# Kernel tuning notes

Hardware: AMD Instinct MI355X
Metric: run time of the kernel (lower is better)

Reference implementation:

```python
import jax, jax.numpy as jnp
import numpy as np

TEMPERATURE = 0.5
EPS = 1e-20


def setup_inputs() -> dict:
    key = jax.random.key(0)
    ks = jax.random.split(key, 7)
    N, T, S = 16, 64, 1024
    SRC, TGT, D = 512, 512, 64
    return {
        "input": jax.random.normal(ks[0], (N, T, TGT), jnp.float32),
        "memory_bank": jax.random.normal(ks[1], (N, S, SRC), jnp.float32),
        "W_q": jax.random.normal(ks[2], (TGT, D), jnp.float32) / np.sqrt(TGT),
        "W_ctx": jax.random.normal(ks[3], (SRC, D), jnp.float32) / np.sqrt(SRC),
        "v": jax.random.normal(ks[4], (D,), jnp.float32) / np.sqrt(D),
        "W_out": jax.random.normal(ks[5], (SRC + TGT, TGT), jnp.float32) / np.sqrt(SRC + TGT),
        "b_out": jax.random.normal(ks[6], (TGT,), jnp.float32) * 0.01,
    }


def reference(input, memory_bank, W_q, W_ctx, v, W_out, b_out):
    # MLP attention score: v^T tanh(W_q q + W_ctx h)
    wq = jnp.einsum("ntd,de->nte", input, W_q)            # [N,T,D]
    uh = jnp.einsum("nsd,de->nse", memory_bank, W_ctx)    # [N,S,D]
    wquh = jnp.tanh(wq[:, :, None, :] + uh[:, None, :, :])  # [N,T,S,D]
    scores = jnp.einsum("ntsd,d->nts", wquh, v)           # [N,T,S]

    log_alpha = jax.nn.log_softmax(scores, axis=-1)
    alpha = jnp.exp(log_alpha)                            # c_align_vectors

    # deterministic context + output
    context_c = jnp.einsum("nts,nsd->ntd", alpha, memory_bank)
    h_c = jnp.tanh(jnp.concatenate([input, context_c], axis=-1) @ W_out + b_out)

    # gumbel-softmax sample (K = n_samples = 1, forced by view_as in original)
    u = jax.random.uniform(jax.random.key(42), log_alpha.shape, jnp.float32)
    g = -jnp.log(-jnp.log(u + EPS) + EPS)                 # gumbel noise
    y_align = jax.nn.softmax((log_alpha + g) / TEMPERATURE, axis=-1)  # [N,T,S]

    context_y = jnp.einsum("nts,nsd->ntd", y_align, memory_bank)
    h_y = jnp.tanh(jnp.concatenate([input, context_y], axis=-1) @ W_out + b_out)

    return jnp.stack([h_c, h_y], axis=0)  # [2,N,T,tgt_dim]
```

## Files before the change

### kernel.cpp

```cpp
#include <hip/hip_runtime.h>
#include <hip/hip_bf16.h>
#include <stdint.h>

#define DEV __device__ __forceinline__

typedef __attribute__((ext_vector_type(8))) short short8;
typedef __attribute__((ext_vector_type(4))) float f32x4;

#define TWO_LOG2E 2.8853900817779268f

DEV unsigned short f2bf(float f) {
  uint32_t u = __float_as_uint(f);
  u += 0x7FFFu + ((u >> 16) & 1u);
  return (unsigned short)(u >> 16);
}

DEV uint2 pk4(float4 f) {
  union { __hip_bfloat162 h; unsigned u; } a, b;
  a.h = __float22bfloat162_rn(make_float2(f.x, f.y));
  b.h = __float22bfloat162_rn(make_float2(f.z, f.w));
  return make_uint2(a.u, b.u);
}

DEV short8 mk8(uint2 lo, uint2 hi) {
  union { short8 s; uint4 u; } t;
  t.u = make_uint4(lo.x, lo.y, hi.x, hi.y);
  return t.s;
}

DEV uint32_t rotl32(uint32_t x, int r) { return (x << r) | (x >> (32 - r)); }

DEV void threefry_0_42(uint32_t x0, uint32_t x1, uint32_t& o0, uint32_t& o1) {
  const uint32_t ks0 = 0u, ks1 = 42u, ks2 = 0x1BD11BDAu ^ 42u;
  x0 += ks0; x1 += ks1;
#define TFR(r) { x0 += x1; x1 = rotl32(x1, (r)); x1 ^= x0; }
  TFR(13) TFR(15) TFR(26) TFR(6)  x0 += ks1; x1 += ks2 + 1u;
  TFR(17) TFR(29) TFR(16) TFR(24) x0 += ks2; x1 += ks0 + 2u;
  TFR(13) TFR(15) TFR(26) TFR(6)  x0 += ks0; x1 += ks1 + 3u;
  TFR(17) TFR(29) TFR(16) TFR(24) x0 += ks1; x1 += ks2 + 4u;
  TFR(13) TFR(15) TFR(26) TFR(6)  x0 += ks2; x1 += ks0 + 5u;
#undef TFR
  o0 = x0; o1 = x1;
}

DEV float wredmax(float v) {
#pragma unroll
  for (int off = 32; off > 0; off >>= 1) v = fmaxf(v, __shfl_xor(v, off));
  return v;
}
DEV float wredsum(float v) {
#pragma unroll
  for (int off = 32; off > 0; off >>= 1) v += __shfl_xor(v, off);
  return v;
}

DEV void ph_transpose(int b, int tid, char* smem,
                      const float* Wctx, const float* Wq, const float* Wout,
                      unsigned short* WctxT, unsigned short* WqT, unsigned short* WoutT) {
  float (*tile)[65] = (float(*)[65])smem;
  const float* src; unsigned short* dst; int R, C, br, bc;
  if (b < 8)       { src = Wctx; dst = WctxT; R = 512;  C = 64;  br = b * 64;       bc = 0; }
  else if (b < 16) { src = Wq;   dst = WqT;   R = 512;  C = 64;  br = (b - 8) * 64; bc = 0; }
  else { int i = b - 16; src = Wout; dst = WoutT; R = 1024; C = 512; br = (i & 15) * 64; bc = (i >> 4) * 64; }
  const int lr = tid >> 4, lc4 = (tid & 15) * 4;
#pragma unroll
  for (int i = 0; i < 4; ++i) {
    float4 vv = *(const float4*)(src + (long)(br + lr + i * 16) * C + bc + lc4);
    tile[lr + i * 16][lc4 + 0] = vv.x;
    tile[lr + i * 16][lc4 + 1] = vv.y;
    tile[lr + i * 16][lc4 + 2] = vv.z;
    tile[lr + i * 16][lc4 + 3] = vv.w;
  }
  __syncthreads();
#pragma unroll
  for (int i = 0; i < 4; ++i) {
    int crow = lr + i * 16;
    ushort4 o;
    o.x = f2bf(tile[lc4 + 0][crow]);
    o.y = f2bf(tile[lc4 + 1][crow]);
    o.z = f2bf(tile[lc4 + 2][crow]);
    o.w = f2bf(tile[lc4 + 3][crow]);
    *(ushort4*)(dst + (long)(bc + crow) * R + br + lc4) = o;
  }
}

DEV void ph_mbtile(int i, int tid, char* smem, const float* mb, unsigned short* mbT) {
  float (*tile)[65] = (float(*)[65])smem;
  const int n = i >> 7, rem = i & 127;
  const int sr0 = (rem >> 3) * 64;
  const int c0 = (rem & 7) * 64;
  const int lr = tid >> 4, lc4 = (tid & 15) * 4;
#pragma unroll
  for (int k = 0; k < 4; ++k) {
    float4 vv = *(const float4*)(mb + ((long)n * 1024 + sr0 + lr + k * 16) * 512 + c0 + lc4);
    tile[lr + k * 16][lc4 + 0] = vv.x;
    tile[lr + k * 16][lc4 + 1] = vv.y;
    tile[lr + k * 16][lc4 + 2] = vv.z;
    tile[lr + k * 16][lc4 + 3] = vv.w;
  }
  __syncthreads();
#pragma unroll
  for (int k = 0; k < 4; ++k) {
    int crow = lr + k * 16;
    ushort4 o;
    o.x = f2bf(tile[lc4 + 0][crow]);
    o.y = f2bf(tile[lc4 + 1][crow]);
    o.z = f2bf(tile[lc4 + 2][crow]);
    o.w = f2bf(tile[lc4 + 3][crow]);
    *(ushort4*)(mbT + (long)n * 524288 + (long)(c0 + crow) * 1024 + sr0 + lc4) = o;
  }
}

DEV void ph_uhwq(int t, int tid, char* smem,
                 const float* mb, const float* input,
                 const unsigned short* WctxT, const unsigned short* WqT,
                 float* uhT, float* wqo) {
  unsigned short (*As)[32] = (unsigned short(*)[32])smem;
  unsigned short (*Bs)[32] = (unsigned short(*)[32])(smem + 4096);
  const float* A; const unsigned short* BT; int mbase;
  if (t < 256) { A = mb;    BT = WctxT; mbase = t * 64; }
  else         { A = input; BT = WqT;   mbase = (t - 256) * 64; }
  const int srow = tid >> 2, kc = tid & 3;
  const int scol = ((kc ^ (srow & 3)) * 8);
  const int wave = tid >> 6, lane = tid & 63;
  const int wm = (wave >> 1) * 32, wn = (wave & 1) * 32;
  const int q = lane >> 4, r = lane & 15;
  const int c0 = ((q ^ (r & 3)) * 8);
  const float* ap = A + (long)(mbase + srow) * 512 + kc * 8;
  const unsigned short* bp = BT + (long)srow * 512 + kc * 8;
  f32x4 acc[2][2];
#pragma unroll
  for (int i = 0; i < 2; ++i)
#pragma unroll
    for (int j = 0; j < 2; ++j) acc[i][j] = (f32x4){0.f, 0.f, 0.f, 0.f};
  float4 fa0 = *(const float4*)(ap);
  float4 fa1 = *(const float4*)(ap + 4);
  uint4 fb = *(const uint4*)(bp);
  for (int k0 = 0; k0 < 512; k0 += 32) {
    uint2 p0 = pk4(fa0), p1 = pk4(fa1);
    *(uint4*)&As[srow][scol] = make_uint4(p0.x, p0.y, p1.x, p1.y);
    *(uint4*)&Bs[srow][scol] = fb;
    __syncthreads();
    if (k0 + 32 < 512) {
      fa0 = *(const float4*)(ap + k0 + 32);
      fa1 = *(const float4*)(ap + k0 + 36);
      fb = *(const uint4*)(bp + k0 + 32);
    }
    short8 a0 = *(const short8*)&As[wm + r][c0];
    short8 a1 = *(const short8*)&As[wm + 16 + r][c0];
    short8 b0 = *(const short8*)&Bs[wn + r][c0];
    short8 b1 = *(const short8*)&Bs[wn + 16 + r][c0];
    acc[0][0] = __builtin_amdgcn_mfma_f32_16x16x32_bf16(a0, b0, acc[0][0], 0, 0, 0);
    acc[0][1] = __builtin_amdgcn_mfma_f32_16x16x32_bf16(a0, b1, acc[0][1], 0, 0, 0);
    acc[1][0] = __builtin_amdgcn_mfma_f32_16x16x32_bf16(a1, b0, acc[1][0], 0, 0, 0);
    acc[1][1] = __builtin_amdgcn_mfma_f32_16x16x32_bf16(a1, b1, acc[1][1], 0, 0, 0);
    __syncthreads();
  }
#pragma unroll
  for (int i2 = 0; i2 < 2; ++i2)
#pragma unroll
    for (int j2 = 0; j2 < 2; ++j2) {
      int gcol = wn + j2 * 16 + r;
      int m = mbase + wm + i2 * 16 + q * 4;
      if (t < 256) {
        int n = m >> 10, s0 = m & 1023;
        float4 o;
        o.x = acc[i2][j2][0] * TWO_LOG2E;
        o.y = acc[i2][j2][1] * TWO_LOG2E;
        o.z = acc[i2][j2][2] * TWO_LOG2E;
        o.w = acc[i2][j2][3] * TWO_LOG2E;
        *(float4*)(uhT + (long)n * 65536 + (long)gcol * 1024 + s0) = o;
      } else {
#pragma unroll
        for (int reg = 0; reg < 4; ++reg)
          wqo[(long)(m + reg) * 64 + gcol] = acc[i2][j2][reg] * TWO_LOG2E;
      }
    }
}

DEV void ph_pre(int tt, int tid, char* smem,
                const float* input, const unsigned short* WoutT,
                const float* bout, float* P) {
  unsigned short (*As)[32] = (unsigned short(*)[32])smem;
  unsigned short (*Bs)[32] = (unsigned short(*)[32])(smem + 4096);
  const int mbase = (tt >> 4) * 64, nbase = (tt & 15) * 32;
  const int srow = tid >> 2, kc = tid & 3;
  const int scol = ((kc ^ (srow & 3)) * 8);
  const int wave = tid >> 6, lane = tid & 63;
  const int wm = (wave >> 1) * 32, wn = (wave & 1) * 16;
  const int q = lane >> 4, r = lane & 15;
  const int c0 = ((q ^ (r & 3)) * 8);
  const float* ap = input + (long)(mbase + srow) * 512 + kc * 8;
  const int brow = (tid & 127) >> 2;
  const unsigned short* bp = WoutT + (long)(nbase + brow) * 1024 + kc * 8;
  f32x4 acc[2];
  acc[0] = (f32x4){0.f, 0.f, 0.f, 0.f};
  acc[1] = (f32x4){0.f, 0.f, 0.f, 0.f};
  float4 fa0 = *(const float4*)(ap);
  float4 fa1 = *(const float4*)(ap + 4);
  uint4 fb;
  if (tid < 128) fb = *(const uint4*)(bp);
  for (int k0 = 0; k0 < 512; k0 += 32) {
    uint2 p0 = pk4(fa0), p1 = pk4(fa1);
    *(uint4*)&As[srow][scol] = make_uint4(p0.x, p0.y, p1.x, p1.y);
    if (tid < 128) *(uint4*)&Bs[brow][(kc ^ (brow & 3)) * 8] = fb;
    __syncthreads();
    int kn = k0 + 32;
    if (kn < 512) {
      fa0 = *(const float4*)(ap + kn);
      fa1 = *(const float4*)(ap + kn + 4);
      if (tid < 128) fb = *(const uint4*)(bp + kn);
    }
    short8 a0 = *(const short8*)&As[wm + r][c0];
    short8 a1 = *(const short8*)&As[wm + 16 + r][c0];
    short8 b0 = *(const short8*)&Bs[wn + r][c0];
    acc[0] = __builtin_amdgcn_mfma_f32_16x16x32_bf16(a0, b0, acc[0], 0, 0, 0);
    acc[1] = __builtin_amdgcn_mfma_f32_16x16x32_bf16(a1, b0, acc[1], 0, 0, 0);
    __syncthreads();
  }
#pragma unroll
  for (int i2 = 0; i2 < 2; ++i2) {
    int gcol = nbase + wn + r;
    float bb = bout[gcol];
#pragma unroll
    for (int reg = 0; reg < 4; ++reg) {
      int grow = mbase + wm + i2 * 16 + q * 4 + reg;
      P[(long)grow * 512 + gcol] = acc[i2][reg] + bb;
    }
  }
}

DEV void softmax_gumbel_write(float* lsc, int nt, int tid, float* red,
                              unsigned short* alpha_bf, unsigned short* yal_bf) {
  const int wv = tid >> 6, ln = tid & 63;
  float m = fmaxf(fmaxf(lsc[0], lsc[1]), fmaxf(lsc[2], lsc[3]));
  m = wredmax(m);
  if (ln == 0) red[wv] = m;
  __syncthreads();
  m = fmaxf(fmaxf(red[0], red[1]), fmaxf(red[2], red[3]));
  __syncthreads();
  float ss = 0.f;
#pragma unroll
  for (int i = 0; i < 4; ++i) ss += __expf(lsc[i] - m);
  ss = wredsum(ss);
  if (ln == 0) red[wv] = ss;
  __syncthreads();
  ss = red[0] + red[1] + red[2] + red[3];
  const float logl = __logf(ss);
  __syncthreads();

  const uint32_t jbase = (uint32_t)nt * 1024u + (uint32_t)tid * 4u;
  float ys[4];
  float4 av;
#pragma unroll
  for (int i = 0; i < 4; ++i) {
    float la = lsc[i] - m - logl;
    ((float*)&av)[i] = __expf(la);
    uint32_t o0, o1;
    threefry_0_42(0u, jbase + i, o0, o1);
    uint32_t bits = o0 ^ o1;
    float u = __uint_as_float((bits >> 9) | 0x3f800000u) - 1.0f;
    float g = -__logf(-__logf(u + 1e-20f) + 1e-20f);
    ys[i] = (la + g) * 2.0f;
  }
  {
    uint2 pa = pk4(av);
    *(uint2*)(alpha_bf + (long)nt * 1024 + tid * 4) = pa;
  }
  float m2 = fmaxf(fmaxf(ys[0], ys[1]), fmaxf(ys[2], ys[3]));
  m2 = wredmax(m2);
  if (ln == 0) red[wv] = m2;
  __syncthreads();
  m2 = fmaxf(fmaxf(red[0], red[1]), fmaxf(red[2], red[3]));
  __syncthreads();
  float s2 = 0.f;
  float4 ye;
#pragma unroll
  for (int i = 0; i < 4; ++i) { ((float*)&ye)[i] = __expf(ys[i] - m2); s2 += ((float*)&ye)[i]; }
  s2 = wredsum(s2);
  if (ln == 0) red[wv] = s2;
  __syncthreads();
  s2 = red[0] + red[1] + red[2] + red[3];
  const float rinv = __fdividef(1.f, s2);
  ye.x *= rinv; ye.y *= rinv; ye.z *= rinv; ye.w *= rinv;
  {
    uint2 py = pk4(ye);
    *(uint2*)(yal_bf + (long)nt * 1024 + tid * 4) = py;
  }
  __syncthreads();
}

DEV void ph_scores_pair(int nt0, int tid, char* smem,
                        const float* uhT, const float* wqo, const float* vvec,
                        unsigned short* alpha_bf, unsigned short* yal_bf) {
  float* wvs0 = (float*)smem;
  float* wvs1 = wvs0 + 64;
  float* vvs  = wvs1 + 64;
  float* red  = vvs + 64;
  const int nt1 = nt0 + 512;
  const int n0 = nt0 >> 6, n1 = nt1 >> 6;
  if (tid < 64) {
    wvs0[tid] = wqo[nt0 * 64 + tid];
    wvs1[tid] = wqo[nt1 * 64 + tid];
    vvs[tid]  = vvec[tid];
  }
  __syncthreads();
  float sumv = 0.f;
#pragma unroll
  for (int d = 0; d < 64; d += 4) {
    float4 vv = *(const float4*)&vvs[d];
    sumv += vv.x + vv.y + vv.z + vv.w;
  }
  const float* un0 = uhT + (long)n0 * 65536 + tid * 4;
  const float* un1 = uhT + (long)n1 * 65536 + tid * 4;
  float4 r0 = make_float4(0.f, 0.f, 0.f, 0.f);
  float4 r1 = make_float4(0.f, 0.f, 0.f, 0.f);
  for (int db = 0; db < 64; db += 4) {
    float4 ua[4], ub[4];
#pragma unroll
    for (int j = 0; j < 4; ++j) {
      ua[j] = *(const float4*)(un0 + (long)(db + j) * 1024);
      ub[j] = *(const float4*)(un1 + (long)(db + j) * 1024);
    }
#pragma unroll
    for (int j = 0; j < 4; ++j) {
      float w0 = wvs0[db + j], w1 = wvs1[db + j], vvj = vvs[db + j];
      r0.x = fmaf(vvj, __builtin_amdgcn_rcpf(1.f + __builtin_amdgcn_exp2f(ua[j].x + w0)), r0.x);
      r0.y = fmaf(vvj, __builtin_amdgcn_rcpf(1.f + __builtin_amdgcn_exp2f(ua[j].y + w0)), r0.y);
      r0.z = fmaf(vvj, __builtin_amdgcn_rcpf(1.f + __builtin_amdgcn_exp2f(ua[j].z + w0)), r0.z);
      r0.w = fmaf(vvj, __builtin_amdgcn_rcpf(1.f + __builtin_amdgcn_exp2f(ua[j].w + w0)), r0.w);
      r1.x = fmaf(vvj, __builtin_amdgcn_rcpf(1.f + __builtin_amdgcn_exp2f(ub[j].x + w1)), r1.x);
      r1.y = fmaf(vvj, __builtin_amdgcn_rcpf(1.f + __builtin_amdgcn_exp2f(ub[j].y + w1)), r1.y);
      r1.z = fmaf(vvj, __builtin_amdgcn_rcpf(1.f + __builtin_amdgcn_exp2f(ub[j].z + w1)), r1.z);
      r1.w = fmaf(vvj, __builtin_amdgcn_rcpf(1.f + __builtin_amdgcn_exp2f(ub[j].w + w1)), r1.w);
    }
  }
  float lsc0[4], lsc1[4];
  lsc0[0] = fmaf(-2.f, r0.x, sumv); lsc0[1] = fmaf(-2.f, r0.y, sumv);
  lsc0[2] = fmaf(-2.f, r0.z, sumv); lsc0[3] = fmaf(-2.f, r0.w, sumv);
  lsc1[0] = fmaf(-2.f, r1.x, sumv); lsc1[1] = fmaf(-2.f, r1.y, sumv);
  lsc1[2] = fmaf(-2.f, r1.z, sumv); lsc1[3] = fmaf(-2.f, r1.w, sumv);
  softmax_gumbel_write(lsc0, nt0, tid, red, alpha_bf, yal_bf);
  softmax_gumbel_write(lsc1, nt1, tid, red, alpha_bf, yal_bf);
}

DEV void ph_ctx_fast(int n, int dbase, int vt, int tid, char* smem,
                     const unsigned short* alpha_bf, const unsigned short* yal_bf,
                     const unsigned short* mbT, unsigned short* ctxb) {
  unsigned short (*As)[32] = (unsigned short(*)[32])smem;
  const int srow = tid >> 2, kc = tid & 3;
  const int scol = ((kc ^ (srow & 3)) * 8);
  const int wave = tid >> 6, lane = tid & 63;
  const int wm = (wave >> 1) * 32, wn = (wave & 1) * 16;
  const int q = lane >> 4, r = lane & 15;
  const int c0 = ((q ^ (r & 3)) * 8);
  const unsigned short* Ab = (vt ? yal_bf : alpha_bf) + (long)n * 65536 + (long)srow * 1024 + kc * 8;
  const unsigned short* Bb = mbT + (long)n * 524288 + (long)(dbase + wn + r) * 1024 + q * 8;
  f32x4 acc[2];
  acc[0] = (f32x4){0.f, 0.f, 0.f, 0.f};
  acc[1] = (f32x4){0.f, 0.f, 0.f, 0.f};
  uint4 fa  = *(const uint4*)(Ab);
  uint4 fb0 = *(const uint4*)(Bb);
  uint4 fb1 = *(const uint4*)(Bb + 32);
  for (int k0 = 0; k0 < 1024; k0 += 32) {
    *(uint4*)&As[srow][scol] = fa;
    __syncthreads();
    union { uint4 u; short8 s; } bu; bu.u = fb0;
    if (k0 + 32 < 1024) fa = *(const uint4*)(Ab + k0 + 32);
    fb0 = fb1;
    if (k0 + 64 < 1024) fb1 = *(const uint4*)(Bb + k0 + 64);
    short8 a0 = *(const short8*)&As[wm + r][c0];
    short8 a1 = *(const short8*)&As[wm + 16 + r][c0];
    acc[0] = __builtin_amdgcn_mfma_f32_16x16x32_bf16(a0, bu.s, acc[0], 0, 0, 0);
    acc[1] = __builtin_amdgcn_mfma_f32_16x16x32_bf16(a1, bu.s, acc[1], 0, 0, 0);
    __syncthreads();
  }
#pragma unroll
  for (int i2 = 0; i2 < 2; ++i2) {
    int gcol = dbase + wn + r;
#pragma unroll
    for (int reg = 0; reg < 4; ++reg) {
      long grow = (long)vt * 1024 + n * 64 + wm + i2 * 16 + q * 4 + reg;
      ctxb[grow * 512 + gcol] = f2bf(acc[i2][reg]);
    }
  }
}

DEV void ph_ctx_legacy(int n, int dbase, int vt, int tid, char* smem,
                       const unsigned short* alpha_bf, const unsigned short* yal_bf,
                       const float* mb, unsigned short* ctxb) {
  unsigned short (*As)[32] = (unsigned short(*)[32])smem;
  const int srow = tid >> 2, kc = tid & 3;
  const int scol = ((kc ^ (srow & 3)) * 8);
  const int wave = tid >> 6, lane = tid & 63;
  const int wm = (wave >> 1) * 32, wn = (wave & 1) * 16;
  const int q = lane >> 4, r = lane & 15;
  const int c0 = ((q ^ (r & 3)) * 8);
  const unsigned short* Ab = (vt ? yal_bf : alpha_bf) + (long)n * 65536 + (long)srow * 1024 + kc * 8;
  const float* bcol = mb + (long)n * 524288 + dbase + wn + r;
  f32x4 acc[2];
  acc[0] = (f32x4){0.f, 0.f, 0.f, 0.f};
  acc[1] = (f32x4){0.f, 0.f, 0.f, 0.f};
  uint4 fa = *(const uint4*)(Ab);
  float bv[8];
#pragma unroll
  for (int j = 0; j < 8; ++j) bv[j] = bcol[(long)(q * 8 + j) * 512];
  for (int k0 = 0; k0 < 1024; k0 += 32) {
    *(uint4*)&As[srow][scol] = fa;
    __syncthreads();
    float4 blo = make_float4(bv[0], bv[1], bv[2], bv[3]);
    float4 bhi = make_float4(bv[4], bv[5], bv[6], bv[7]);
    short8 b0 = mk8(pk4(blo), pk4(bhi));
    if (k0 + 32 < 1024) {
      fa = *(const uint4*)(Ab + k0 + 32);
#pragma unroll
      for (int j = 0; j < 8; ++j) bv[j] = bcol[(long)(k0 + 32 + q * 8 + j) * 512];
    }
    short8 a0 = *(const short8*)&As[wm + r][c0];
    short8 a1 = *(const short8*)&As[wm + 16 + r][c0];
    acc[0] = __builtin_amdgcn_mfma_f32_16x16x32_bf16(a0, b0, acc[0], 0, 0, 0);
    acc[1] = __builtin_amdgcn_mfma_f32_16x16x32_bf16(a1, b0, acc[1], 0, 0, 0);
    __syncthreads();
  }
#pragma unroll
  for (int i2 = 0; i2 < 2; ++i2) {
    int gcol = dbase + wn + r;
#pragma unroll
    for (int reg = 0; reg < 4; ++reg) {
      long grow = (long)vt * 1024 + n * 64 + wm + i2 * 16 + q * 4 + reg;
      ctxb[grow * 512 + gcol] = f2bf(acc[i2][reg]);
    }
  }
}

DEV void ph_out(int mbase, int nbase, int tid, char* smem,
                const unsigned short* ctxb, const unsigned short* WoutT,
                const float* P, float* out) {
  unsigned short (*As)[32] = (unsigned short(*)[32])smem;
  unsigned short (*Bs)[32] = (unsigned short(*)[32])(smem + 4096);
  const int srow = tid >> 2, kc = tid & 3;
  const int scol = ((kc ^ (srow & 3)) * 8);
  const int wave = tid >> 6, lane = tid & 63;
  const int wm = (wave >> 1) * 32, wn = (wave & 1) * 16;
  const int q = lane >> 4, r = lane & 15;
  const int c0 = ((q ^ (r & 3)) * 8);
  const unsigned short* ap = ctxb + (long)(mbase + srow) * 512 + kc * 8;
  const int brow = (tid & 127) >> 2;
  const unsigned short* bp = WoutT + (long)(nbase + brow) * 1024 + 512 + kc * 8;
  f32x4 acc[2];
#pragma unroll
  for (int i2 = 0; i2 < 2; ++i2) {
    int pcol = nbase + wn + r;
#pragma unroll
    for (int reg = 0; reg < 4; ++reg) {
      int prow = (mbase + wm + i2 * 16 + q * 4 + reg) & 1023;
      acc[i2][reg] = P[(long)prow * 512 + pcol];
    }
  }
  uint4 fa = *(const uint4*)(ap);
  uint4 fb;
  if (tid < 128) fb = *(const uint4*)(bp);
  for (int k0 = 0; k0 < 512; k0 += 32) {
    *(uint4*)&As[srow][scol] = fa;
    if (tid < 128) *(uint4*)&Bs[brow][(kc ^ (brow & 3)) * 8] = fb;
    __syncthreads();
    int kn = k0 + 32;
    if (kn < 512) {
      fa = *(const uint4*)(ap + kn);
      if (tid < 128) fb = *(const uint4*)(bp + kn);
    }
    short8 a0 = *(const short8*)&As[wm + r][c0];
    short8 a1 = *(const short8*)&As[wm + 16 + r][c0];
    short8 b0 = *(const short8*)&Bs[wn + r][c0];
    acc[0] = __builtin_amdgcn_mfma_f32_16x16x32_bf16(a0, b0, acc[0], 0, 0, 0);
    acc[1] = __builtin_amdgcn_mfma_f32_16x16x32_bf16(a1, b0, acc[1], 0, 0, 0);
    __syncthreads();
  }
#pragma unroll
  for (int i2 = 0; i2 < 2; ++i2) {
    int gcol = nbase + wn + r;
#pragma unroll
    for (int reg = 0; reg < 4; ++reg) {
      int grow = mbase + wm + i2 * 16 + q * 4 + reg;
      float z = acc[i2][reg];
      float rc = __builtin_amdgcn_rcpf(1.f + __builtin_amdgcn_exp2f(z * TWO_LOG2E));
      out[(long)grow * 512 + gcol] = fmaf(-2.f, rc, 1.f);
    }
  }
}

__global__ __launch_bounds__(256) void k_prep(const float* __restrict__ Wctx,
                                              const float* __restrict__ Wq,
                                              const float* __restrict__ Wout,
                                              const float* __restrict__ mb,
                                              unsigned short* __restrict__ WctxT,
                                              unsigned short* __restrict__ WqT,
                                              unsigned short* __restrict__ WoutT,
                                              unsigned short* __restrict__ mbT) {
  __shared__ __align__(16) char smem[16640];
  const int b = blockIdx.x;
  if (b < 144) ph_transpose(b, threadIdx.x, smem, Wctx, Wq, Wout, WctxT, WqT, WoutT);
  else         ph_mbtile(b - 144, threadIdx.x, smem, mb, mbT);
}

__global__ __launch_bounds__(256) void k_uhwq_pre(const float* __restrict__ mb,
                                                  const float* __restrict__ input,
                                                  const unsigned short* __restrict__ WctxT,
                                                  const unsigned short* __restrict__ WqT,
                                                  const unsigned short* __restrict__ WoutT,
                                                  const float* __restrict__ bout,
                                                  float* __restrict__ uhT,
                                                  float* __restrict__ wqo,
                                                  float* __restrict__ P) {
  __shared__ __align__(16) char smem[8192];
  const int b = blockIdx.x;
  if (b < 272) ph_uhwq(b, threadIdx.x, smem, mb, input, WctxT, WqT, uhT, wqo);
  else         ph_pre(b - 272, threadIdx.x, smem, input, WoutT, bout, P);
}

__global__ __launch_bounds__(256) void k_scores(const float* __restrict__ uhT,
                                                const float* __restrict__ wqo,
                                                const float* __restrict__ vvec,
                                                unsigned short* __restrict__ alpha_bf,
                                                unsigned short* __restrict__ yal_bf) {
  __shared__ __align__(16) char smem[1024];
  ph_scores_pair(blockIdx.x, threadIdx.x, smem, uhT, wqo, vvec, alpha_bf, yal_bf);
}

__global__ __launch_bounds__(256) void k_ctx_fast(const unsigned short* __restrict__ alpha_bf,
                                                  const unsigned short* __restrict__ yal_bf,
                                                  const unsigned short* __restrict__ mbT,
                                                  unsigned short* __restrict__ ctxb) {
  __shared__ __align__(16) char smem[4096];
  const int x = blockIdx.x;
  ph_ctx_fast(x & 15, ((x >> 4) & 15) * 32, x >> 8, threadIdx.x, smem, alpha_bf, yal_bf, mbT, ctxb);
}

__global__ __launch_bounds__(256) void k_ctx_legacy(const unsigned short* __restrict__ alpha_bf,
                                                    const unsigned short* __restrict__ yal_bf,
                                                    const float* __restrict__ mb,
                                                    unsigned short* __restrict__ ctxb) {
  __shared__ __align__(16) char smem[4096];
  const int x = blockIdx.x;
  ph_ctx_legacy(x & 15, ((x >> 4) & 15) * 32, x >> 8, threadIdx.x, smem, alpha_bf, yal_bf, mb, ctxb);
}

__global__ __launch_bounds__(256) void k_out(const unsigned short* __restrict__ ctxb,
                                             const unsigned short* __restrict__ WoutT,
                                             const float* __restrict__ P,
                                             float* __restrict__ out) {
  __shared__ __align__(16) char smem[8192];
  ph_out((blockIdx.x >> 4) * 64, (blockIdx.x & 15) * 32, threadIdx.x, smem, ctxb, WoutT, P, out);
}

extern "C" void kernel_launch(void* const* d_in, const int* in_sizes, int n_in,
                              void* d_out, int out_size, void* d_ws, size_t ws_size,
                              hipStream_t stream) {
  const float* input = (const float*)d_in[0];
  const float* mb    = (const float*)d_in[1];
  const float* W_q   = (const float*)d_in[2];
  const float* W_ctx = (const float*)d_in[3];
  const float* v     = (const float*)d_in[4];
  const float* W_out = (const float*)d_in[5];
  const float* b_out = (const float*)d_in[6];
  float* out = (float*)d_out;
  float* ws = (float*)d_ws;

  float* uhT = ws;
  float* wqo = ws + 1048576;
  unsigned short* alpha_bf = (unsigned short*)(ws + 1114112);
  unsigned short* yal_bf   = (unsigned short*)(ws + 1638400);
  unsigned short* WctxT = (unsigned short*)(ws + 2162688);
  unsigned short* WqT   = (unsigned short*)(ws + 2179072);
  unsigned short* WoutT = (unsigned short*)(ws + 2195456);
  unsigned short* ctxb  = (unsigned short*)(ws + 2457600);
  float* P = ws + 2981888;
  unsigned short* mbT = (unsigned short*)(ws + 3506176);

  const bool big = ws_size >= (size_t)7700480 * 4;

  k_prep<<<big ? 2192 : 144, 256, 0, stream>>>(W_ctx, W_q, W_out, mb, WctxT, WqT, WoutT, mbT);
  k_uhwq_pre<<<528, 256, 0, stream>>>(mb, input, WctxT, WqT, WoutT, b_out, uhT, wqo, P);
  k_scores<<<512, 256, 0, stream>>>(uhT, wqo, v, alpha_bf, yal_bf);
  if (big) k_ctx_fast<<<512, 256, 0, stream>>>(alpha_bf, yal_bf, mbT, ctxb);
  else     k_ctx_legacy<<<512, 256, 0, stream>>>(alpha_bf, yal_bf, mb, ctxb);
  k_out<<<512, 256, 0, stream>>>(ctxb, WoutT, P, out);
}
```

Before: 147.6 us.

## Pre-convert inputs to bf16 and load MFMA fragments directly from global memory

The prep kernel now also writes bf16 copies of memory_bank and input. New GEMM variants for uh/wq, the output pre-projection, the context GEMM and the output GEMM read MFMA operands straight from global memory with register prefetch, replacing the LDS staging and block barriers. The aim is less fp32 traffic and fewer syncs in the GEMM phases. The cost is a larger workspace requirement and more global-memory writes in prep. Without that workspace, the old paths are used.

```diff
diff --git a/kernel.cpp b/kernel.cpp
--- a/kernel.cpp
+++ b/kernel.cpp
@@ -84,7 +84,8 @@
   }
 }
 
-DEV void ph_mbtile(int i, int tid, char* smem, const float* mb, unsigned short* mbT) {
+DEV void ph_mbtile(int i, int tid, char* smem, const float* mb,
+                   unsigned short* mbT, unsigned short* mb_bf) {
   float (*tile)[65] = (float(*)[65])smem;
   const int n = i >> 7, rem = i & 127;
   const int sr0 = (rem >> 3) * 64;
@@ -92,11 +93,15 @@
   const int lr = tid >> 4, lc4 = (tid & 15) * 4;
 #pragma unroll
   for (int k = 0; k < 4; ++k) {
-    float4 vv = *(const float4*)(mb + ((long)n * 1024 + sr0 + lr + k * 16) * 512 + c0 + lc4);
+    const long srow = (long)n * 1024 + sr0 + lr + k * 16;
+    float4 vv = *(const float4*)(mb + srow * 512 + c0 + lc4);
     tile[lr + k * 16][lc4 + 0] = vv.x;
     tile[lr + k * 16][lc4 + 1] = vv.y;
     tile[lr + k * 16][lc4 + 2] = vv.z;
     tile[lr + k * 16][lc4 + 3] = vv.w;
+    ushort4 o;
+    o.x = f2bf(vv.x); o.y = f2bf(vv.y); o.z = f2bf(vv.z); o.w = f2bf(vv.w);
+    *(ushort4*)(mb_bf + srow * 512 + c0 + lc4) = o;
   }
   __syncthreads();
 #pragma unroll
@@ -108,6 +113,197 @@
     o.z = f2bf(tile[lc4 + 2][crow]);
     o.w = f2bf(tile[lc4 + 3][crow]);
     *(ushort4*)(mbT + (long)n * 524288 + (long)(c0 + crow) * 1024 + sr0 + lc4) = o;
+  }
+}
+
+DEV void ph_inpconv(int i, int tid, const float* input, unsigned short* input_bf) {
+  const long base = (long)i * 8192 + (long)tid * 32;
+#pragma unroll
+  for (int j = 0; j < 32; j += 4) {
+    float4 vv = *(const float4*)(input + base + j);
+    uint2 p = pk4(vv);
+    *(uint2*)(input_bf + base + j) = p;
+  }
+}
+
+DEV void ph_uhwq_fast(int t, int tid,
+                      const unsigned short* mb_bf, const unsigned short* input_bf,
+                      const unsigned short* WctxT, const unsigned short* WqT,
+                      float* uhT, float* wqo) {
+  const unsigned short* A; const unsigned short* BT; int mbase;
+  if (t < 256) { A = mb_bf;    BT = WctxT; mbase = t * 64; }
+  else         { A = input_bf; BT = WqT;   mbase = (t - 256) * 64; }
+  const int wave = tid >> 6, lane = tid & 63;
+  const int wm = (wave >> 1) * 32, wn = (wave & 1) * 32;
+  const int q = lane >> 4, r = lane & 15;
+  const unsigned short* a0p = A + (long)(mbase + wm + r) * 512 + q * 8;
+  const unsigned short* a1p = a0p + 16 * 512;
+  const unsigned short* b0p = BT + (long)(wn + r) * 512 + q * 8;
+  const unsigned short* b1p = b0p + 16 * 512;
+  f32x4 acc[2][2];
+#pragma unroll
+  for (int i = 0; i < 2; ++i)
+#pragma unroll
+    for (int j = 0; j < 2; ++j) acc[i][j] = (f32x4){0.f, 0.f, 0.f, 0.f};
+  uint4 na0 = *(const uint4*)(a0p);
+  uint4 na1 = *(const uint4*)(a1p);
+  uint4 nb0 = *(const uint4*)(b0p);
+  uint4 nb1 = *(const uint4*)(b1p);
+  for (int k0 = 0; k0 < 512; k0 += 32) {
+    union { uint4 u; short8 s; } A0, A1, B0, B1;
+    A0.u = na0; A1.u = na1; B0.u = nb0; B1.u = nb1;
+    if (k0 + 32 < 512) {
+      na0 = *(const uint4*)(a0p + k0 + 32);
+      na1 = *(const uint4*)(a1p + k0 + 32);
+      nb0 = *(const uint4*)(b0p + k0 + 32);
+      nb1 = *(const uint4*)(b1p + k0 + 32);
+    }
+    acc[0][0] = __builtin_amdgcn_mfma_f32_16x16x32_bf16(A0.s, B0.s, acc[0][0], 0, 0, 0);
+    acc[0][1] = __builtin_amdgcn_mfma_f32_16x16x32_bf16(A0.s, B1.s, acc[0][1], 0, 0, 0);
+    acc[1][0] = __builtin_amdgcn_mfma_f32_16x16x32_bf16(A1.s, B0.s, acc[1][0], 0, 0, 0);
+    acc[1][1] = __builtin_amdgcn_mfma_f32_16x16x32_bf16(A1.s, B1.s, acc[1][1], 0, 0, 0);
+  }
+#pragma unroll
+  for (int i2 = 0; i2 < 2; ++i2)
+#pragma unroll
+    for (int j2 = 0; j2 < 2; ++j2) {
+      int gcol = wn + j2 * 16 + r;
+      int m = mbase + wm + i2 * 16 + q * 4;
+      if (t < 256) {
+        int n = m >> 10, s0 = m & 1023;
+        float4 o;
+        o.x = acc[i2][j2][0] * TWO_LOG2E;
+        o.y = acc[i2][j2][1] * TWO_LOG2E;
+        o.z = acc[i2][j2][2] * TWO_LOG2E;
+        o.w = acc[i2][j2][3] * TWO_LOG2E;
+        *(float4*)(uhT + (long)n * 65536 + (long)gcol * 1024 + s0) = o;
+      } else {
+#pragma unroll
+        for (int reg = 0; reg < 4; ++reg)
+          wqo[(long)(m + reg) * 64 + gcol] = acc[i2][j2][reg] * TWO_LOG2E;
+      }
+    }
+}
+
+DEV void ph_pre_fast(int tt, int tid, const unsigned short* input_bf,
+                     const unsigned short* WoutT, const float* bout, float* P) {
+  const int mbase = (tt >> 4) * 64, nbase = (tt & 15) * 32;
+  const int wave = tid >> 6, lane = tid & 63;
+  const int wm = (wave >> 1) * 32, wn = (wave & 1) * 16;
+  const int q = lane >> 4, r = lane & 15;
+  const unsigned short* a0p = input_bf + (long)(mbase + wm + r) * 512 + q * 8;
+  const unsigned short* a1p = a0p + 16 * 512;
+  const unsigned short* bp  = WoutT + (long)(nbase + wn + r) * 1024 + q * 8;
+  f32x4 acc[2];
+  acc[0] = (f32x4){0.f, 0.f, 0.f, 0.f};
+  acc[1] = (f32x4){0.f, 0.f, 0.f, 0.f};
+  uint4 na0 = *(const uint4*)(a0p);
+  uint4 na1 = *(const uint4*)(a1p);
+  uint4 nb  = *(const uint4*)(bp);
+  for (int k0 = 0; k0 < 512; k0 += 32) {
+    union { uint4 u; short8 s; } A0, A1, B0;
+    A0.u = na0; A1.u = na1; B0.u = nb;
+    if (k0 + 32 < 512) {
+      na0 = *(const uint4*)(a0p + k0 + 32);
+      na1 = *(const uint4*)(a1p + k0 + 32);
+      nb  = *(const uint4*)(bp + k0 + 32);
+    }
+    acc[0] = __builtin_amdgcn_mfma_f32_16x16x32_bf16(A0.s, B0.s, acc[0], 0, 0, 0);
+    acc[1] = __builtin_amdgcn_mfma_f32_16x16x32_bf16(A1.s, B0.s, acc[1], 0, 0, 0);
+  }
+#pragma unroll
+  for (int i2 = 0; i2 < 2; ++i2) {
+    int gcol = nbase + wn + r;
+    float bb = bout[gcol];
+#pragma unroll
+    for (int reg = 0; reg < 4; ++reg) {
+      int grow = mbase + wm + i2 * 16 + q * 4 + reg;
+      P[(long)grow * 512 + gcol] = acc[i2][reg] + bb;
+    }
+  }
+}
+
+DEV void ph_ctx_fast2(int n, int dbase, int vt, int tid,
+                      const unsigned short* alpha_bf, const unsigned short* yal_bf,
+                      const unsigned short* mbT, unsigned short* ctxb) {
+  const int wave = tid >> 6, lane = tid & 63;
+  const int wm = (wave >> 1) * 32, wn = (wave & 1) * 16;
+  const int q = lane >> 4, r = lane & 15;
+  const unsigned short* Abase = (vt ? yal_bf : alpha_bf) + (long)n * 65536;
+  const unsigned short* a0p = Abase + (long)(wm + r) * 1024 + q * 8;
+  const unsigned short* a1p = a0p + 16 * 1024;
+  const unsigned short* bp  = mbT + (long)n * 524288 + (long)(dbase + wn + r) * 1024 + q * 8;
+  f32x4 acc[2];
+  acc[0] = (f32x4){0.f, 0.f, 0.f, 0.f};
+  acc[1] = (f32x4){0.f, 0.f, 0.f, 0.f};
+  uint4 na0 = *(const uint4*)(a0p);
+  uint4 na1 = *(const uint4*)(a1p);
+  uint4 nb  = *(const uint4*)(bp);
+  for (int k0 = 0; k0 < 1024; k0 += 32) {
+    union { uint4 u; short8 s; } A0, A1, B0;
+    A0.u = na0; A1.u = na1; B0.u = nb;
+    if (k0 + 32 < 1024) {
+      na0 = *(const uint4*)(a0p + k0 + 32);
+      na1 = *(const uint4*)(a1p + k0 + 32);
+      nb  = *(const uint4*)(bp + k0 + 32);
+    }
+    acc[0] = __builtin_amdgcn_mfma_f32_16x16x32_bf16(A0.s, B0.s, acc[0], 0, 0, 0);
+    acc[1] = __builtin_amdgcn_mfma_f32_16x16x32_bf16(A1.s, B0.s, acc[1], 0, 0, 0);
+  }
+#pragma unroll
+  for (int i2 = 0; i2 < 2; ++i2) {
+    int gcol = dbase + wn + r;
+#pragma unroll
+    for (int reg = 0; reg < 4; ++reg) {
+      long grow = (long)vt * 1024 + n * 64 + wm + i2 * 16 + q * 4 + reg;
+      ctxb[grow * 512 + gcol] = f2bf(acc[i2][reg]);
+    }
+  }
+}
+
+DEV void ph_out_fast(int mbase, int nbase, int tid,
+                     const unsigned short* ctxb, const unsigned short* WoutT,
+                     const float* P, float* out) {
+  const int wave = tid >> 6, lane = tid & 63;
+  const int wm = (wave >> 1) * 32, wn = (wave & 1) * 16;
+  const int q = lane >> 4, r = lane & 15;
+  const unsigned short* a0p = ctxb + (long)(mbase + wm + r) * 512 + q * 8;
+  const unsigned short* a1p = a0p + 16 * 512;
+  const unsigned short* bp  = WoutT + (long)(nbase + wn + r) * 1024 + 512 + q * 8;
+  f32x4 acc[2];
+#pragma unroll
+  for (int i2 = 0; i2 < 2; ++i2) {
+    int pcol = nbase + wn + r;
+#pragma unroll
+    for (int reg = 0; reg < 4; ++reg) {
+      int prow = (mbase + wm + i2 * 16 + q * 4 + reg) & 1023;
+      acc[i2][reg] = P[(long)prow * 512 + pcol];
+    }
+  }
+  uint4 na0 = *(const uint4*)(a0p);
+  uint4 na1 = *(const uint4*)(a1p);
+  uint4 nb  = *(const uint4*)(bp);
+  for (int k0 = 0; k0 < 512; k0 += 32) {
+    union { uint4 u; short8 s; } A0, A1, B0;
+    A0.u = na0; A1.u = na1; B0.u = nb;
+    if (k0 + 32 < 512) {
+      na0 = *(const uint4*)(a0p + k0 + 32);
+      na1 = *(const uint4*)(a1p + k0 + 32);
+      nb  = *(const uint4*)(bp + k0 + 32);
+    }
+    acc[0] = __builtin_amdgcn_mfma_f32_16x16x32_bf16(A0.s, B0.s, acc[0], 0, 0, 0);
+    acc[1] = __builtin_amdgcn_mfma_f32_16x16x32_bf16(A1.s, B0.s, acc[1], 0, 0, 0);
+  }
+#pragma unroll
+  for (int i2 = 0; i2 < 2; ++i2) {
+    int gcol = nbase + wn + r;
+#pragma unroll
+    for (int reg = 0; reg < 4; ++reg) {
+      int grow = mbase + wm + i2 * 16 + q * 4 + reg;
+      float z = acc[i2][reg];
+      float rc = __builtin_amdgcn_rcpf(1.f + __builtin_amdgcn_exp2f(z * TWO_LOG2E));
+      out[(long)grow * 512 + gcol] = fmaf(-2.f, rc, 1.f);
+    }
   }
 }
 
@@ -230,162 +426,6 @@
   }
 }
 
-DEV void softmax_gumbel_write(float* lsc, int nt, int tid, float* red,
-                              unsigned short* alpha_bf, unsigned short* yal_bf) {
-  const int wv = tid >> 6, ln = tid & 63;
-  float m = fmaxf(fmaxf(lsc[0], lsc[1]), fmaxf(lsc[2], lsc[3]));
-  m = wredmax(m);
-  if (ln == 0) red[wv] = m;
-  __syncthreads();
-  m = fmaxf(fmaxf(red[0], red[1]), fmaxf(red[2], red[3]));
-  __syncthreads();
-  float ss = 0.f;
-#pragma unroll
-  for (int i = 0; i < 4; ++i) ss += __expf(lsc[i] - m);
-  ss = wredsum(ss);
-  if (ln == 0) red[wv] = ss;
-  __syncthreads();
-  ss = red[0] + red[1] + red[2] + red[3];
-  const float logl = __logf(ss);
-  __syncthreads();
-
-  const uint32_t jbase = (uint32_t)nt * 1024u + (uint32_t)tid * 4u;
-  float ys[4];
-  float4 av;
-#pragma unroll
-  for (int i = 0; i < 4; ++i) {
-    float la = lsc[i] - m - logl;
-    ((float*)&av)[i] = __expf(la);
-    uint32_t o0, o1;
-    threefry_0_42(0u, jbase + i, o0, o1);
-    uint32_t bits = o0 ^ o1;
-    float u = __uint_as_float((bits >> 9) | 0x3f800000u) - 1.0f;
-    float g = -__logf(-__logf(u + 1e-20f) + 1e-20f);
-    ys[i] = (la + g) * 2.0f;
-  }
-  {
-    uint2 pa = pk4(av);
-    *(uint2*)(alpha_bf + (long)nt * 1024 + tid * 4) = pa;
-  }
-  float m2 = fmaxf(fmaxf(ys[0], ys[1]), fmaxf(ys[2], ys[3]));
-  m2 = wredmax(m2);
-  if (ln == 0) red[wv] = m2;
-  __syncthreads();
-  m2 = fmaxf(fmaxf(red[0], red[1]), fmaxf(red[2], red[3]));
-  __syncthreads();
-  float s2 = 0.f;
-  float4 ye;
-#pragma unroll
-  for (int i = 0; i < 4; ++i) { ((float*)&ye)[i] = __expf(ys[i] - m2); s2 += ((float*)&ye)[i]; }
-  s2 = wredsum(s2);
-  if (ln == 0) red[wv] = s2;
-  __syncthreads();
-  s2 = red[0] + red[1] + red[2] + red[3];
-  const float rinv = __fdividef(1.f, s2);
-  ye.x *= rinv; ye.y *= rinv; ye.z *= rinv; ye.w *= rinv;
-  {
-    uint2 py = pk4(ye);
-    *(uint2*)(yal_bf + (long)nt * 1024 + tid * 4) = py;
-  }
-  __syncthreads();
-}
-
-DEV void ph_scores_pair(int nt0, int tid, char* smem,
-                        const float* uhT, const float* wqo, const float* vvec,
-                        unsigned short* alpha_bf, unsigned short* yal_bf) {
-  float* wvs0 = (float*)smem;
-  float* wvs1 = wvs0 + 64;
-  float* vvs  = wvs1 + 64;
-  float* red  = vvs + 64;
-  const int nt1 = nt0 + 512;
-  const int n0 = nt0 >> 6, n1 = nt1 >> 6;
-  if (tid < 64) {
-    wvs0[tid] = wqo[nt0 * 64 + tid];
-    wvs1[tid] = wqo[nt1 * 64 + tid];
-    vvs[tid]  = vvec[tid];
-  }
-  __syncthreads();
-  float sumv = 0.f;
-#pragma unroll
-  for (int d = 0; d < 64; d += 4) {
-    float4 vv = *(const float4*)&vvs[d];
-    sumv += vv.x + vv.y + vv.z + vv.w;
-  }
-  const float* un0 = uhT + (long)n0 * 65536 + tid * 4;
-  const float* un1 = uhT + (long)n1 * 65536 + tid * 4;
-  float4 r0 = make_float4(0.f, 0.f, 0.f, 0.f);
-  float4 r1 = make_float4(0.f, 0.f, 0.f, 0.f);
-  for (int db = 0; db < 64; db += 4) {
-    float4 ua[4], ub[4];
-#pragma unroll
-    for (int j = 0; j < 4; ++j) {
-      ua[j] = *(const float4*)(un0 + (long)(db + j) * 1024);
-      ub[j] = *(const float4*)(un1 + (long)(db + j) * 1024);
-    }
-#pragma unroll
-    for (int j = 0; j < 4; ++j) {
-      float w0 = wvs0[db + j], w1 = wvs1[db + j], vvj = vvs[db + j];
-      r0.x = fmaf(vvj, __builtin_amdgcn_rcpf(1.f + __builtin_amdgcn_exp2f(ua[j].x + w0)), r0.x);
-      r0.y = fmaf(vvj, __builtin_amdgcn_rcpf(1.f + __builtin_amdgcn_exp2f(ua[j].y + w0)), r0.y);
-      r0.z = fmaf(vvj, __builtin_amdgcn_rcpf(1.f + __builtin_amdgcn_exp2f(ua[j].z + w0)), r0.z);
-      r0.w = fmaf(vvj, __builtin_amdgcn_rcpf(1.f + __builtin_amdgcn_exp2f(ua[j].w + w0)), r0.w);
-      r1.x = fmaf(vvj, __builtin_amdgcn_rcpf(1.f + __builtin_amdgcn_exp2f(ub[j].x + w1)), r1.x);
-      r1.y = fmaf(vvj, __builtin_amdgcn_rcpf(1.f + __builtin_amdgcn_exp2f(ub[j].y + w1)), r1.y);
-      r1.z = fmaf(vvj, __builtin_amdgcn_rcpf(1.f + __builtin_amdgcn_exp2f(ub[j].z + w1)), r1.z);
-      r1.w = fmaf(vvj, __builtin_amdgcn_rcpf(1.f + __builtin_amdgcn_exp2f(ub[j].w + w1)), r1.w);
-    }
-  }
-  float lsc0[4], lsc1[4];
-  lsc0[0] = fmaf(-2.f, r0.x, sumv); lsc0[1] = fmaf(-2.f, r0.y, sumv);
-  lsc0[2] = fmaf(-2.f, r0.z, sumv); lsc0[3] = fmaf(-2.f, r0.w, sumv);
-  lsc1[0] = fmaf(-2.f, r1.x, sumv); lsc1[1] = fmaf(-2.f, r1.y, sumv);
-  lsc1[2] = fmaf(-2.f, r1.z, sumv); lsc1[3] = fmaf(-2.f, r1.w, sumv);
-  softmax_gumbel_write(lsc0, nt0, tid, red, alpha_bf, yal_bf);
-  softmax_gumbel_write(lsc1, nt1, tid, red, alpha_bf, yal_bf);
-}
-
-DEV void ph_ctx_fast(int n, int dbase, int vt, int tid, char* smem,
-                     const unsigned short* alpha_bf, const unsigned short* yal_bf,
-                     const unsigned short* mbT, unsigned short* ctxb) {
-  unsigned short (*As)[32] = (unsigned short(*)[32])smem;
-  const int srow = tid >> 2, kc = tid & 3;
-  const int scol = ((kc ^ (srow & 3)) * 8);
-  const int wave = tid >> 6, lane = tid & 63;
-  const int wm = (wave >> 1) * 32, wn = (wave & 1) * 16;
-  const int q = lane >> 4, r = lane & 15;
-  const int c0 = ((q ^ (r & 3)) * 8);
-  const unsigned short* Ab = (vt ? yal_bf : alpha_bf) + (long)n * 65536 + (long)srow * 1024 + kc * 8;
-  const unsigned short* Bb = mbT + (long)n * 524288 + (long)(dbase + wn + r) * 1024 + q * 8;
-  f32x4 acc[2];
-  acc[0] = (f32x4){0.f, 0.f, 0.f, 0.f};
-  acc[1] = (f32x4){0.f, 0.f, 0.f, 0.f};
-  uint4 fa  = *(const uint4*)(Ab);
-  uint4 fb0 = *(const uint4*)(Bb);
-  uint4 fb1 = *(const uint4*)(Bb + 32);
-  for (int k0 = 0; k0 < 1024; k0 += 32) {
-    *(uint4*)&As[srow][scol] = fa;
-    __syncthreads();
-    union { uint4 u; short8 s; } bu; bu.u = fb0;
-    if (k0 + 32 < 1024) fa = *(const uint4*)(Ab + k0 + 32);
-    fb0 = fb1;
-    if (k0 + 64 < 1024) fb1 = *(const uint4*)(Bb + k0 + 64);
-    short8 a0 = *(const short8*)&As[wm + r][c0];
-    short8 a1 = *(const short8*)&As[wm + 16 + r][c0];
-    acc[0] = __builtin_amdgcn_mfma_f32_16x16x32_bf16(a0, bu.s, acc[0], 0, 0, 0);
-    acc[1] = __builtin_amdgcn_mfma_f32_16x16x32_bf16(a1, bu.s, acc[1], 0, 0, 0);
-    __syncthreads();
-  }
-#pragma unroll
-  for (int i2 = 0; i2 < 2; ++i2) {
-    int gcol = dbase + wn + r;
-#pragma unroll
-    for (int reg = 0; reg < 4; ++reg) {
-      long grow = (long)vt * 1024 + n * 64 + wm + i2 * 16 + q * 4 + reg;
-      ctxb[grow * 512 + gcol] = f2bf(acc[i2][reg]);
-    }
-  }
-}
-
 DEV void ph_ctx_legacy(int n, int dbase, int vt, int tid, char* smem,
                        const unsigned short* alpha_bf, const unsigned short* yal_bf,
                        const float* mb, unsigned short* ctxb) {
@@ -489,18 +529,150 @@
   }
 }
 
+DEV void softmax_gumbel_write(float* lsc, int nt, int tid, float* red,
+                              unsigned short* alpha_bf, unsigned short* yal_bf) {
+  const int wv = tid >> 6, ln = tid & 63;
+  float m = fmaxf(fmaxf(lsc[0], lsc[1]), fmaxf(lsc[2], lsc[3]));
+  m = wredmax(m);
+  if (ln == 0) red[wv] = m;
+  __syncthreads();
+  m = fmaxf(fmaxf(red[0], red[1]), fmaxf(red[2], red[3]));
+  __syncthreads();
+  float ss = 0.f;
+#pragma unroll
+  for (int i = 0; i < 4; ++i) ss += __expf(lsc[i] - m);
+  ss = wredsum(ss);
+  if (ln == 0) red[wv] = ss;
+  __syncthreads();
+  ss = red[0] + red[1] + red[2] + red[3];
+  const float logl = __logf(ss);
+  __syncthreads();
+
+  const uint32_t jbase = (uint32_t)nt * 1024u + (uint32_t)tid * 4u;
+  float ys[4];
+  float4 av;
+#pragma unroll
+  for (int i = 0; i < 4; ++i) {
+    float la = lsc[i] - m - logl;
+    ((float*)&av)[i] = __expf(la);
+    uint32_t o0, o1;
+    threefry_0_42(0u, jbase + i, o0, o1);
+    uint32_t bits = o0 ^ o1;
+    float u = __uint_as_float((bits >> 9) | 0x3f800000u) - 1.0f;
+    float g = -__logf(-__logf(u + 1e-20f) + 1e-20f);
+    ys[i] = (la + g) * 2.0f;
+  }
+  {
+    uint2 pa = pk4(av);
+    *(uint2*)(alpha_bf + (long)nt * 1024 + tid * 4) = pa;
+  }
+  float m2 = fmaxf(fmaxf(ys[0], ys[1]), fmaxf(ys[2], ys[3]));
+  m2 = wredmax(m2);
+  if (ln == 0) red[wv] = m2;
+  __syncthreads();
+  m2 = fmaxf(fmaxf(red[0], red[1]), fmaxf(red[2], red[3]));
+  __syncthreads();
+  float s2 = 0.f;
+  float4 ye;
+#pragma unroll
+  for (int i = 0; i < 4; ++i) { ((float*)&ye)[i] = __expf(ys[i] - m2); s2 += ((float*)&ye)[i]; }
+  s2 = wredsum(s2);
+  if (ln == 0) red[wv] = s2;
+  __syncthreads();
+  s2 = red[0] + red[1] + red[2] + red[3];
+  const float rinv = __fdividef(1.f, s2);
+  ye.x *= rinv; ye.y *= rinv; ye.z *= rinv; ye.w *= rinv;
+  {
+    uint2 py = pk4(ye);
+    *(uint2*)(yal_bf + (long)nt * 1024 + tid * 4) = py;
+  }
+  __syncthreads();
+}
+
+DEV void ph_scores_pair(int nt0, int tid, char* smem,
+                        const float* uhT, const float* wqo, const float* vvec,
+                        unsigned short* alpha_bf, unsigned short* yal_bf) {
+  float* wvs0 = (float*)smem;
+  float* wvs1 = wvs0 + 64;
+  float* vvs  = wvs1 + 64;
+  float* red  = vvs + 64;
+  const int nt1 = nt0 + 512;
+  const int n0 = nt0 >> 6, n1 = nt1 >> 6;
+  if (tid < 64) {
+    wvs0[tid] = wqo[nt0 * 64 + tid];
+    wvs1[tid] = wqo[nt1 * 64 + tid];
+    vvs[tid]  = vvec[tid];
+  }
+  __syncthreads();
+  float sumv = 0.f;
+#pragma unroll
+  for (int d = 0; d < 64; d += 4) {
+    float4 vv = *(const float4*)&vvs[d];
+    sumv += vv.x + vv.y + vv.z + vv.w;
+  }
+  const float* un0 = uhT + (long)n0 * 65536 + tid * 4;
+  const float* un1 = uhT + (long)n1 * 65536 + tid * 4;
+  float4 r0 = make_float4(0.f, 0.f, 0.f, 0.f);
+  float4 r1 = make_float4(0.f, 0.f, 0.f, 0.f);
+  for (int db = 0; db < 64; db += 4) {
+    float4 ua[4], ub[4];
+#pragma unroll
+    for (int j = 0; j < 4; ++j) {
+      ua[j] = *(const float4*)(un0 + (long)(db + j) * 1024);
+      ub[j] = *(const float4*)(un1 + (long)(db + j) * 1024);
+    }
+#pragma unroll
+    for (int j = 0; j < 4; ++j) {
+      float w0 = wvs0[db + j], w1 = wvs1[db + j], vvj = vvs[db + j];
+      r0.x = fmaf(vvj, __builtin_amdgcn_rcpf(1.f + __builtin_amdgcn_exp2f(ua[j].x + w0)), r0.x);
+      r0.y = fmaf(vvj, __builtin_amdgcn_rcpf(1.f + __builtin_amdgcn_exp2f(ua[j].y + w0)), r0.y);
+      r0.z = fmaf(vvj, __builtin_amdgcn_rcpf(1.f + __builtin_amdgcn_exp2f(ua[j].z + w0)), r0.z);
+      r0.w = fmaf(vvj, __builtin_amdgcn_rcpf(1.f + __builtin_amdgcn_exp2f(ua[j].w + w0)), r0.w);
+      r1.x = fmaf(vvj, __builtin_amdgcn_rcpf(1.f + __builtin_amdgcn_exp2f(ub[j].x + w1)), r1.x);
+      r1.y = fmaf(vvj, __builtin_amdgcn_rcpf(1.f + __builtin_amdgcn_exp2f(ub[j].y + w1)), r1.y);
+      r1.z = fmaf(vvj, __builtin_amdgcn_rcpf(1.f + __builtin_amdgcn_exp2f(ub[j].z + w1)), r1.z);
+      r1.w = fmaf(vvj, __builtin_amdgcn_rcpf(1.f + __builtin_amdgcn_exp2f(ub[j].w + w1)), r1.w);
+    }
+  }
+  float lsc0[4], lsc1[4];
+  lsc0[0] = fmaf(-2.f, r0.x, sumv); lsc0[1] = fmaf(-2.f, r0.y, sumv);
+  lsc0[2] = fmaf(-2.f, r0.z, sumv); lsc0[3] = fmaf(-2.f, r0.w, sumv);
+  lsc1[0] = fmaf(-2.f, r1.x, sumv); lsc1[1] = fmaf(-2.f, r1.y, sumv);
+  lsc1[2] = fmaf(-2.f, r1.z, sumv); lsc1[3] = fmaf(-2.f, r1.w, sumv);
+  softmax_gumbel_write(lsc0, nt0, tid, red, alpha_bf, yal_bf);
+  softmax_gumbel_write(lsc1, nt1, tid, red, alpha_bf, yal_bf);
+}
+
 __global__ __launch_bounds__(256) void k_prep(const float* __restrict__ Wctx,
                                               const float* __restrict__ Wq,
                                               const float* __restrict__ Wout,
                                               const float* __restrict__ mb,
+                                              const float* __restrict__ input,
                                               unsigned short* __restrict__ WctxT,
                                               unsigned short* __restrict__ WqT,
                                               unsigned short* __restrict__ WoutT,
-                                              unsigned short* __restrict__ mbT) {
+                                              unsigned short* __restrict__ mbT,
+                                              unsigned short* __restrict__ mb_bf,
+                                              unsigned short* __restrict__ input_bf) {
   __shared__ __align__(16) char smem[16640];
   const int b = blockIdx.x;
-  if (b < 144) ph_transpose(b, threadIdx.x, smem, Wctx, Wq, Wout, WctxT, WqT, WoutT);
-  else         ph_mbtile(b - 144, threadIdx.x, smem, mb, mbT);
+  if (b < 144)       ph_transpose(b, threadIdx.x, smem, Wctx, Wq, Wout, WctxT, WqT, WoutT);
+  else if (b < 2192) ph_mbtile(b - 144, threadIdx.x, smem, mb, mbT, mb_bf);
+  else               ph_inpconv(b - 2192, threadIdx.x, input, input_bf);
+}
+
+__global__ __launch_bounds__(256) void k_uhwq_pre_fast(const unsigned short* __restrict__ mb_bf,
+                                                       const unsigned short* __restrict__ input_bf,
+                                                       const unsigned short* __restrict__ WctxT,
+                                                       const unsigned short* __restrict__ WqT,
+                                                       const unsigned short* __restrict__ WoutT,
+                                                       const float* __restrict__ bout,
+                                                       float* __restrict__ uhT,
+                                                       float* __restrict__ wqo,
+                                                       float* __restrict__ P) {
+  const int b = blockIdx.x;
+  if (b < 272) ph_uhwq_fast(b, threadIdx.x, mb_bf, input_bf, WctxT, WqT, uhT, wqo);
+  else         ph_pre_fast(b - 272, threadIdx.x, input_bf, WoutT, bout, P);
 }
 
 __global__ __launch_bounds__(256) void k_uhwq_pre(const float* __restrict__ mb,
@@ -527,13 +699,12 @@
   ph_scores_pair(blockIdx.x, threadIdx.x, smem, uhT, wqo, vvec, alpha_bf, yal_bf);
 }
 
-__global__ __launch_bounds__(256) void k_ctx_fast(const unsigned short* __restrict__ alpha_bf,
-                                                  const unsigned short* __restrict__ yal_bf,
-                                                  const unsigned short* __restrict__ mbT,
-                                                  unsigned short* __restrict__ ctxb) {
-  __shared__ __align__(16) char smem[4096];
+__global__ __launch_bounds__(256) void k_ctx_fast2(const unsigned short* __restrict__ alpha_bf,
+                                                   const unsigned short* __restrict__ yal_bf,
+                                                   const unsigned short* __restrict__ mbT,
+                                                   unsigned short* __restrict__ ctxb) {
   const int x = blockIdx.x;
-  ph_ctx_fast(x & 15, ((x >> 4) & 15) * 32, x >> 8, threadIdx.x, smem, alpha_bf, yal_bf, mbT, ctxb);
+  ph_ctx_fast2(x & 15, ((x >> 4) & 15) * 32, x >> 8, threadIdx.x, alpha_bf, yal_bf, mbT, ctxb);
 }
 
 __global__ __launch_bounds__(256) void k_ctx_legacy(const unsigned short* __restrict__ alpha_bf,
@@ -543,6 +714,13 @@
   __shared__ __align__(16) char smem[4096];
   const int x = blockIdx.x;
   ph_ctx_legacy(x & 15, ((x >> 4) & 15) * 32, x >> 8, threadIdx.x, smem, alpha_bf, yal_bf, mb, ctxb);
+}
+
+__global__ __launch_bounds__(256) void k_out_fast(const unsigned short* __restrict__ ctxb,
+                                                  const unsigned short* __restrict__ WoutT,
+                                                  const float* __restrict__ P,
+                                                  float* __restrict__ out) {
+  ph_out_fast((blockIdx.x >> 4) * 64, (blockIdx.x & 15) * 32, threadIdx.x, ctxb, WoutT, P, out);
 }
 
 __global__ __launch_bounds__(256) void k_out(const unsigned short* __restrict__ ctxb,
@@ -575,14 +753,20 @@
   unsigned short* WoutT = (unsigned short*)(ws + 2195456);
   unsigned short* ctxb  = (unsigned short*)(ws + 2457600);
   float* P = ws + 2981888;
-  unsigned short* mbT = (unsigned short*)(ws + 3506176);
-
-  const bool big = ws_size >= (size_t)7700480 * 4;
-
-  k_prep<<<big ? 2192 : 144, 256, 0, stream>>>(W_ctx, W_q, W_out, mb, WctxT, WqT, WoutT, mbT);
-  k_uhwq_pre<<<528, 256, 0, stream>>>(mb, input, WctxT, WqT, WoutT, b_out, uhT, wqo, P);
+  unsigned short* mbT      = (unsigned short*)(ws + 3506176);
+  unsigned short* mb_bf    = (unsigned short*)(ws + 7700480);
+  unsigned short* input_bf = (unsigned short*)(ws + 11894784);
+
+  const bool big = ws_size >= (size_t)12156928 * 4;
+
+  k_prep<<<big ? 2256 : 144, 256, 0, stream>>>(W_ctx, W_q, W_out, mb, input,
+                                               WctxT, WqT, WoutT, mbT, mb_bf, input_bf);
+  if (big) k_uhwq_pre_fast<<<528, 256, 0, stream>>>(mb_bf, input_bf, WctxT, WqT, WoutT,
+                                                    b_out, uhT, wqo, P);
+  else     k_uhwq_pre<<<528, 256, 0, stream>>>(mb, input, WctxT, WqT, WoutT, b_out, uhT, wqo, P);
   k_scores<<<512, 256, 0, stream>>>(uhT, wqo, v, alpha_bf, yal_bf);
-  if (big) k_ctx_fast<<<512, 256, 0, stream>>>(alpha_bf, yal_bf, mbT, ctxb);
+  if (big) k_ctx_fast2<<<512, 256, 0, stream>>>(alpha_bf, yal_bf, mbT, ctxb);
   else     k_ctx_legacy<<<512, 256, 0, stream>>>(alpha_bf, yal_bf, mb, ctxb);
-  k_out<<<512, 256, 0, stream>>>(ctxb, WoutT, P, out);
-}
+  if (big) k_out_fast<<<512, 256, 0, stream>>>(ctxb, WoutT, P, out);
+  else     k_out<<<512, 256, 0, stream>>>(ctxb, WoutT, P, out);
+}
```

Measured after the change: 177.7 us. 20.4% more time.
